# Optimization experiments

Measured on AMD Instinct MI355X. Metric: run time of the kernel, lower is better.

The kernel has to match this reference:

```python
import math
import jax, jax.numpy as jnp
import numpy as np
from jax import lax

RAY_START, RAY_END = 0.5, 2.5
N_PLANES = 32

# ---- camera constants (faithful to pose_spherical / fibonacci_sphere / ImagePlanes init) ----

def _pose_spherical_np(theta, phi, radius):
    trans_t = np.array([[1,0,0,0],[0,1,0,0],[0,0,1,radius],[0,0,0,1]], dtype=np.float64)
    p = phi/180.0*np.pi
    rot_phi = np.array([[1,0,0,0],[0,np.cos(p),-np.sin(p),0],[0,np.sin(p),np.cos(p),0],[0,0,0,1]], dtype=np.float64)
    t = theta/180.0*np.pi
    rot_theta = np.array([[np.cos(t),0,-np.sin(t),0],[0,1,0,0],[np.sin(t),0,np.cos(t),0],[0,0,0,1]], dtype=np.float64)
    e = 90.0/180.0*np.pi
    rot_eta = np.array([[np.cos(e),np.sin(e),0,0],[-np.sin(e),np.cos(e),0,0],[0,0,1,0],[0,0,0,1]], dtype=np.float64)
    c2w = rot_eta @ (rot_theta @ (rot_phi @ trans_t))
    return np.array([[-1,0,0,0],[0,0,1,0],[0,1,0,0],[0,0,0,1]], dtype=np.float64) @ c2w

def _fibonacci_sphere(n):
    pts = []
    golden = math.pi*(math.sqrt(5.0)-1.0)
    for i in range(n):
        y = 1 - (i/float(n-1))*2
        r = math.sqrt(1-y*y)
        th = golden*i
        x, z = math.cos(th)*r, math.sin(th)*r
        pts.append((math.atan2(z, math.sqrt(x*x+y*y)), math.atan2(y, x)))
    return pts

_poses = np.stack([_pose_spherical_np(theta, phi, -1.307) for phi, theta in _fibonacci_sphere(N_PLANES)])
_flip = np.diag(np.array([-1.0,1.0,1.0,1.0]))
POSES34 = jnp.asarray(np.stack([np.linalg.inv(p @ _flip)[:3] for p in _poses]).astype(np.float32))  # [32,3,4]
KMAT = jnp.asarray(np.array([[1.0254,0,0.5],[0,1.0254,0.5],[0,0,1]], dtype=np.float32))  # [3,3]

# ---- grid_sample(bilinear, zeros, align_corners=False) ----

def _grid_sample(img, grid):
    # img [C,H,W], grid [P,2] (x,y) in [-1,1] -> [C,P]
    C, H, W = img.shape
    ix = ((grid[:, 0] + 1.0)*W - 1.0)*0.5
    iy = ((grid[:, 1] + 1.0)*H - 1.0)*0.5
    x0 = jnp.floor(ix); y0 = jnp.floor(iy)
    wx1 = ix - x0; wy1 = iy - y0
    def tap(xx, yy, w):
        valid = (xx >= 0) & (xx <= W - 1) & (yy >= 0) & (yy <= H - 1)
        xi = jnp.clip(xx, 0, W - 1).astype(jnp.int32)
        yi = jnp.clip(yy, 0, H - 1).astype(jnp.int32)
        return img[:, yi, xi] * (w*valid)[None, :]
    return (tap(x0, y0, (1-wx1)*(1-wy1)) + tap(x0+1, y0, wx1*(1-wy1))
            + tap(x0, y0+1, (1-wx1)*wy1) + tap(x0+1, y0+1, wx1*wy1))

# ---- ImagePlanes.forward ----

def _image_plane_feats(images, points):
    # images [32,3,H,W], points [P,3] -> [P, 96+64]
    P = points.shape[0]
    ph = jnp.concatenate([points, jnp.ones((P, 1), points.dtype)], axis=1)  # [P,4]
    cam = jnp.einsum('kij,pj->kip', POSES34, ph)            # [32,3,P]
    ps = jnp.einsum('ij,kjp->kip', KMAT, cam)                # [32,3,P]
    pix = jnp.clip(ps[:, :2, :] / ps[:, 2:3, :], 0.0, 1.0)*2.0 - 1.0  # [32,2,P]
    grid = jnp.transpose(pix, (0, 2, 1))                     # [32,P,2]
    feats = jax.vmap(_grid_sample)(images, grid)             # [32,3,P]
    feats = jnp.transpose(feats, (2, 0, 1)).reshape(P, -1)   # [P,96] plane-major
    pixflat = jnp.transpose(grid, (1, 0, 2)).reshape(P, -1)  # [P,64]
    return jnp.concatenate([feats, pixflat], axis=1)

# ---- RenderNetwork.forward (only self.net path is used) ----

def _decode(x, W1, b1, W2, b2):
    h = jax.nn.softplus(x @ W1 + b1)
    o = h @ W2 + b2
    rgb = jax.nn.sigmoid(o[..., 1:])*(1.0 + 2*0.001) - 0.001
    return rgb, o[..., 0:1]

# ---- MipRayMarcher2 ----

def _ray_march(colors, densities, depths):
    deltas = depths[:, :, 1:] - depths[:, :, :-1]
    cm = (colors[:, :, :-1] + colors[:, :, 1:])*0.5
    dm = (densities[:, :, :-1] + densities[:, :, 1:])*0.5
    zm = (depths[:, :, :-1] + depths[:, :, 1:])*0.5
    dm = jax.nn.softplus(dm - 1.0)
    alpha = 1.0 - jnp.exp(-dm*deltas)
    shifted = jnp.concatenate([jnp.ones_like(alpha[:, :, :1]), 1.0 - alpha + 1e-10], axis=2)
    weights = alpha * jnp.cumprod(shifted, axis=2)[:, :, :-1]
    rgb = jnp.sum(weights*cm, axis=2)*2.0 - 1.0
    wtot = jnp.sum(weights, axis=2)
    depth = jnp.sum(weights*zm, axis=2)/wtot
    depth = jnp.clip(jnp.where(jnp.isnan(depth), jnp.inf, depth), jnp.min(depths), jnp.max(depths))
    return rgb, depth, weights

# ---- importance sampling (sample_pdf + maxpool/avgpool smoothing) ----

def _sample_pdf(bins, weights, u, eps=1e-5):
    M = weights.shape[-1]
    weights = weights + eps
    pdf = weights / jnp.sum(weights, -1, keepdims=True)
    cdf = jnp.cumsum(pdf, -1)
    cdf = jnp.concatenate([jnp.zeros_like(cdf[:, :1]), cdf], -1)  # [R,M+1]
    inds = jax.vmap(lambda c, uu: jnp.searchsorted(c, uu, side='right'))(cdf, u)
    below = jnp.maximum(inds - 1, 0)
    above = jnp.minimum(inds, M)
    cdf_b = jnp.take_along_axis(cdf, below, 1)
    cdf_a = jnp.take_along_axis(cdf, above, 1)
    bins_b = jnp.take_along_axis(bins, below, 1)
    bins_a = jnp.take_along_axis(bins, above, 1)
    denom = jnp.where(cdf_a - cdf_b < eps, 1.0, cdf_a - cdf_b)
    return bins_b + (u - cdf_b)/denom*(bins_a - bins_b)

def _sample_importance(z_vals, weights, n_imp, u):
    B, N, S, _ = z_vals.shape
    z = z_vals.reshape(B*N, S)
    w = weights.reshape(B*N, S - 1)
    wp = jnp.pad(w, ((0, 0), (1, 1)), constant_values=-jnp.inf)
    m = jnp.maximum(wp[:, :-1], wp[:, 1:])          # max_pool1d(k=2,s=1,p=1)
    sm = (m[:, :-1] + m[:, 1:])*0.5 + 0.01           # avg_pool1d(k=2,s=1)
    samples = _sample_pdf(z, sm[:, 1:-1], u.reshape(B*N, n_imp))
    return lax.stop_gradient(samples).reshape(B, N, n_imp, 1)

# ---- full ImportanceRenderer.forward ----

def _forward(planes, ray_origins, ray_directions, strat_noise, pdf_u, W1, b1, W2, b2, D, n_imp):
    B, N = ray_origins.shape[0], ray_origins.shape[1]
    H, Wd = planes.shape[-2], planes.shape[-1]
    images = planes.reshape(B, N_PLANES, 3, H, Wd)
    delta = (RAY_END - RAY_START)/(D - 1)
    depths_c = jnp.linspace(RAY_START, RAY_END, D, dtype=planes.dtype).reshape(1, 1, D, 1) + strat_noise*delta

    def run_pass(depths):
        S = depths.shape[2]
        pts = (ray_origins[:, :, None, :] + depths*ray_directions[:, :, None, :]).reshape(B, N*S, 3)
        feats = jax.vmap(_image_plane_feats)(images, pts)  # [B,N*S,160]
        rgb, sigma = _decode(feats, W1, b1, W2, b2)
        return rgb.reshape(B, N, S, 32), sigma.reshape(B, N, S, 1)

    colors_c, dens_c = run_pass(depths_c)
    _, _, w_c = _ray_march(colors_c, dens_c, depths_c)
    depths_f = _sample_importance(depths_c, w_c, n_imp, pdf_u)
    colors_f, dens_f = run_pass(depths_f)

    all_d = jnp.concatenate([depths_c, depths_f], axis=2)
    all_c = jnp.concatenate([colors_c, colors_f], axis=2)
    all_s = jnp.concatenate([dens_c, dens_f], axis=2)
    order = jnp.argsort(all_d[..., 0], axis=2)[..., None]
    all_d = jnp.take_along_axis(all_d, order, axis=2)
    all_c = jnp.take_along_axis(all_c, order, axis=2)
    all_s = jnp.take_along_axis(all_s, order, axis=2)
    rgb_final, depth_final, w = _ray_march(all_c, all_s, all_d)
    return jnp.concatenate([rgb_final, depth_final, jnp.sum(w, axis=2)], axis=-1)  # [B,N,34]


def setup_inputs() -> dict:
    key = jax.random.key(0)
    ks = jax.random.split(key, 7)
    B, N, D, NI, H = 2, 4096, 48, 48, 64
    rd = jax.random.normal(ks[2], (B, N, 3), jnp.float32)
    rd = rd / jnp.linalg.norm(rd, axis=-1, keepdims=True)
    return {
        'planes': jax.random.normal(ks[0], (B, 96, H, H), jnp.float32),
        'ray_origins': jax.random.normal(ks[1], (B, N, 3), jnp.float32)*0.1,
        'ray_directions': rd,
        'strat_noise': jax.random.uniform(ks[3], (B, N, D, 1), jnp.float32),
        'pdf_u': jax.random.uniform(ks[4], (B, N, NI), jnp.float32),
        'W1': jax.random.normal(ks[5], (160, 64), jnp.float32)*0.05,
        'b1': jnp.zeros((64,), jnp.float32),
        'W2': jax.random.normal(ks[6], (64, 33), jnp.float32)*0.05,
        'b2': jnp.zeros((33,), jnp.float32),
        'depth_resolution': 48,
        'N_importance': 48,
    }


def reference(planes, ray_origins, ray_directions, strat_noise, pdf_u, W1, b1, W2, b2, depth_resolution, N_importance):
    return _forward(planes, ray_origins, ray_directions, strat_noise, pdf_u, W1, b1, W2, b2, depth_resolution, N_importance)
```

## Files before the change

kernel.cpp:

```cpp
#include <hip/hip_runtime.h>
#include <math.h>

#define B_   2
#define N_   4096
#define S_   48
#define NPL  32
#define NRAYS (B_*N_)
#define NPTS  (NRAYS*S_)
#define DELTA_ (2.0f/47.0f)
#define NBLK_FUSED (NPTS/256)

#define ST_XS    65
#define ST_YS    66
#define ST_PLANE (ST_YS*ST_XS)
#define SETUP_GRID 258

#define OFF_POSES  0
#define OFF_MINMAX 384
#define OFF_W1E    512
#define OFF_W2E    8704
#define OFF_B2E    10240
#define OFF_ST     16384
#define OFF_DC     1114624
#define OFF_DF     1507840
#define OFF_SC     1901056
#define OFF_SF     2294272
#define OFF_CC     2687488
#define OFF_CF     8978944

typedef __attribute__((ext_vector_type(8))) short short8;
typedef __attribute__((ext_vector_type(4))) float f32x4;
typedef __attribute__((ext_vector_type(2))) float f32x2;

__device__ __forceinline__ float softplus_f(float x) {
    return fmaxf(x, 0.f) + __logf(1.f + __expf(-fabsf(x)));
}
__device__ __forceinline__ float sigmoid_f(float x) {
    return __builtin_amdgcn_rcpf(1.f + __expf(-x));
}
__device__ __forceinline__ unsigned short bf16rne(float x) {
    unsigned u = __float_as_uint(x);
    u += 0x7FFFu + ((u >> 16) & 1u);
    return (unsigned short)(u >> 16);
}
__device__ __forceinline__ unsigned bf16pk(float lo, float hi) {
    return (unsigned)bf16rne(lo) | ((unsigned)bf16rne(hi) << 16);
}
__device__ __forceinline__ float bf2f(unsigned short v) {
    return __uint_as_float(((unsigned)v) << 16);
}
__device__ __forceinline__ float bflo(unsigned u) { return __uint_as_float(u << 16); }
__device__ __forceinline__ float bfhi(unsigned u) { return __uint_as_float(u & 0xffff0000u); }
__device__ __forceinline__ f32x2 unpk2(unsigned u) { return (f32x2){bflo(u), bfhi(u)}; }
__device__ __forceinline__ int div48(int pt) {
    return (int)(((unsigned)(pt >> 4) * 43691u) >> 17);
}

__device__ void mul3(const double* a, const double* b, double* o) {
    for (int i = 0; i < 3; i++)
        for (int j = 0; j < 3; j++) {
            double s = 0.0;
            for (int k = 0; k < 3; k++) s += a[i*3+k]*b[k*3+j];
            o[i*3+j] = s;
        }
}

__global__ __launch_bounds__(256) void k_setup(
    float* ws, const float* __restrict__ W1,
    const float* __restrict__ W2, const float* __restrict__ b2,
    const float* __restrict__ planes, const float* __restrict__ noise)
{
    __shared__ unsigned short texs[3][4096];
    __shared__ float smn[4], smx[4];
    int bid = blockIdx.x;
    int t = threadIdx.x;
    if (bid == 0) {
        if (t < 32) {
            double y = 1.0 - (t/31.0)*2.0;
            double rr = sqrt(fmax(1.0 - y*y, 0.0));
            double golden = M_PI*(sqrt(5.0) - 1.0);
            double th = golden*(double)t;
            double x = cos(th)*rr, z = sin(th)*rr;
            double phi   = atan2(z, sqrt(x*x + y*y));
            double theta = atan2(y, x);
            double p  = phi/180.0*M_PI;
            double tt = theta/180.0*M_PI;
            double e  = 90.0/180.0*M_PI;
            double cp = cos(p), sp = sin(p), ct = cos(tt), st = sin(tt);
            double ce = cos(e), se = sin(e);
            double Ph[9] = {1,0,0,  0,cp,-sp,  0,sp,cp};
            double Th[9] = {ct,0,-st,  0,1,0,  st,0,ct};
            double Et[9] = {ce,se,0,  -se,ce,0,  0,0,1};
            double M3[9] = {-1,0,0,  0,0,1,  0,1,0};
            double A[9], Bm[9], R[9];
            mul3(Th, Ph, A);
            mul3(Et, A, Bm);
            mul3(M3, Bm, R);
            double radius = -1.307;
            double tv0 = radius*R[2], tv1 = radius*R[5], tv2 = radius*R[8];
            double Rf[9] = {-R[0],R[1],R[2], -R[3],R[4],R[5], -R[6],R[7],R[8]};
            float rowv[3][4];
            for (int j = 0; j < 3; j++) {
                double r0 = Rf[0*3+j], r1 = Rf[1*3+j], r2 = Rf[2*3+j];
                rowv[j][0] = (float)r0;
                rowv[j][1] = (float)r1;
                rowv[j][2] = (float)r2;
                rowv[j][3] = (float)(-(r0*tv0 + r1*tv1 + r2*tv2));
            }
            float* P = ws + OFF_POSES + t*12;
            P[0] = rowv[0][0]; P[1] = rowv[1][0];
            P[2] = rowv[0][1]; P[3] = rowv[1][1];
            P[4] = rowv[0][2]; P[5] = rowv[1][2];
            P[6] = rowv[0][3]; P[7] = rowv[1][3];
            P[8] = rowv[2][0]; P[9] = rowv[2][1]; P[10] = rowv[2][2]; P[11] = rowv[2][3];
        }
        unsigned short* w1e = (unsigned short*)(ws + OFF_W1E);
        for (int o = t; o < 64*256; o += 256) {
            int chunk = o >> 9, lane = (o >> 3) & 63, j = o & 7;
            int s = chunk >> 2, nt = chunk & 3, q = lane >> 4, n = lane & 15;
            int nn = nt*16 + n;
            int p = s*4 + q;
            float v = 0.f;
            if (j < 3)      v = W1[(3*p+j)*64 + nn];
            else if (j < 5) v = W1[(96 + 2*p + (j-3))*64 + nn];
            w1e[o] = bf16rne(v);
        }
        unsigned short* w2e = (unsigned short*)(ws + OFF_W2E);
        for (int o = t; o < 6*512; o += 256) {
            int chunk = o >> 9, lane = (o >> 3) & 63, j = o & 7;
            int nt = chunk >> 1, s2 = chunk & 1, q = lane >> 4, n = lane & 15;
            int nn = nt*16 + n;
            int k2 = s2*32 + q*8 + j;
            float v = (nn < 33) ? W2[k2*33 + nn] : 0.f;
            w2e[o] = bf16rne(v);
        }
        for (int idx = t; idx < 48; idx += 256)
            ws[OFF_B2E + idx] = (idx < 33) ? b2[idx] : 0.f;
    } else if (bid == 1) {
        float mn = 1e30f, mx = -1e30f;
        for (int r = t; r < NRAYS; r += 256) {
            float n0  = noise[(size_t)r*48];
            float n47 = noise[(size_t)r*48 + 47];
            mn = fminf(mn, 0.5f + n0*DELTA_);
            mx = fmaxf(mx, 0.5f + 47.f*DELTA_ + n47*DELTA_);
        }
        for (int off = 32; off > 0; off >>= 1) {
            mn = fminf(mn, __shfl_down(mn, off));
            mx = fmaxf(mx, __shfl_down(mx, off));
        }
        if ((t & 63) == 0) { smn[t >> 6] = mn; smx[t >> 6] = mx; }
        __syncthreads();
        if (t == 0) {
            ws[OFF_MINMAX]     = fminf(fminf(smn[0], smn[1]), fminf(smn[2], smn[3]));
            ws[OFF_MINMAX + 1] = fmaxf(fmaxf(smx[0], smx[1]), fmaxf(smx[2], smx[3]));
        }
    } else {
        int idx = bid - 2;
        int bp = idx >> 2, part = idx & 3;
        int b = bp >> 5, p = bp & 31;
        const float* base = planes + ((size_t)b*96 + 3*p)*4096;
        for (int i = t; i < 4096; i += 256) {
            texs[0][i] = bf16rne(base[i]);
            texs[1][i] = bf16rne(base[4096 + i]);
            texs[2][i] = bf16rne(base[8192 + i]);
        }
        __syncthreads();
        uint4* qd = (uint4*)(ws + OFF_ST) + (size_t)bp*ST_PLANE;
        int e0 = part*1073, e1 = min(ST_PLANE, e0 + 1073);
        for (int e = e0 + t; e < e1; e += 256) {
            int y = e / ST_XS, x = e - y*ST_XS;
            int jy = y - 1;
            unsigned a01 = 0, a2 = 0, b01 = 0, b2v = 0;
            if (jy >= 0 && jy <= 63) {
                int jxa = x - 1, jxb = x;
                if (jxa >= 0 && jxa <= 63) {
                    int ti = jy*64 + jxa;
                    a01 = (unsigned)texs[0][ti] | ((unsigned)texs[1][ti] << 16);
                    a2  = (unsigned)texs[2][ti];
                }
                if (jxb <= 63) {
                    int ti = jy*64 + jxb;
                    b01 = (unsigned)texs[0][ti] | ((unsigned)texs[1][ti] << 16);
                    b2v = (unsigned)texs[2][ti];
                }
            }
            qd[e] = make_uint4(a01, a2, b01, b2v);
        }
    }
}

__device__ __forceinline__ void proj_pt(
    const f32x2 Px, const f32x2 Py, const f32x2 Pz, const f32x2 Pw, const f32x4 Pc,
    float px, float py, float pz,
    int& eoff, float& wx, float& wy, unsigned& gpk)
{
    f32x2 c01 = Pz*pz + Pw;
    c01 = Py*py + c01;
    c01 = Px*px + c01;
    float c2 = fmaf(Pc.x,px, fmaf(Pc.y,py, fmaf(Pc.z,pz, Pc.w)));
    float rz = __builtin_amdgcn_rcpf(c2);
    f32x2 t01 = c01*1.0254f + 0.5f*c2;
    t01 = t01*rz;
    float cx = fminf(fmaxf(t01.x, 0.f), 1.f);
    float cy = fminf(fmaxf(t01.y, 0.f), 1.f);
    float gx = fmaf(2.f, cx, -1.f);
    float gy = fmaf(2.f, cy, -1.f);
    float ixp = fmaf(64.f, cx, 0.5f);
    float iyp = fmaf(64.f, cy, 0.5f);
    float xf = floorf(ixp), yf = floorf(iyp);
    wx = ixp - xf; wy = iyp - yf;
    eoff = (int)yf*ST_XS + (int)xf;
    gpk = bf16pk(gx, gy);
}

__device__ __forceinline__ void bilerp_pack(
    const uint4 r0, const uint4 r1, float wx, float wy, unsigned gpk, uint4& av)
{
    float wy0 = 1.f - wy, wy1 = wy;
    float w0x = 1.f - wx, w1x = wx;
    f32x2 tl01 = unpk2(r0.x)*wy0 + unpk2(r1.x)*wy1;
    float tl2  = fmaf(wy0, bflo(r0.y), wy1*bflo(r1.y));
    f32x2 tr01 = unpk2(r0.z)*wy0 + unpk2(r1.z)*wy1;
    float tr2  = fmaf(wy0, bflo(r0.w), wy1*bflo(r1.w));
    f32x2 f01 = tl01*w0x + tr01*w1x;
    float f2  = fmaf(w0x, tl2, w1x*tr2);
    av.x = bf16pk(f01.x, f01.y);
    av.y = ((unsigned)bf16rne(f2)) | (gpk << 16);
    av.z = gpk >> 16;
    av.w = 0u;
}

__global__ __launch_bounds__(512, 4) void k_fused(
    const uint4* __restrict__ stq, const float* __restrict__ poses,
    const float* __restrict__ b1, const unsigned short* __restrict__ w1e,
    const unsigned short* __restrict__ w2e, const float* __restrict__ b2e,
    unsigned short* __restrict__ colors, float* __restrict__ dens,
    const float* __restrict__ noise, const float* __restrict__ ro,
    const float* __restrict__ rd, const float* __restrict__ u,
    float* __restrict__ ws, int coarse)
{
    __shared__ __align__(16) unsigned short w1s[16384];
    __shared__ __align__(16) unsigned short w2s[3072];
    __shared__ __align__(16) unsigned short smem[8][1152];
    __shared__ __align__(16) float pl[384];
    __shared__ float impz[6][48];
    __shared__ float impcdf[6][46];
    __shared__ __align__(16) float4 posl[6][48];
    int tid = threadIdx.x;
    int wv = tid >> 6, lane = tid & 63;
    int n = lane & 15, q = lane >> 4;
    int bid = blockIdx.x;
    int swz = (bid & 7)*(NBLK_FUSED/8) + (bid >> 3);
    int wlocal = swz*256 + wv*32;
    int bq = (swz*256 >= NPTS/2) ? 32 : 0;
    int r0 = (int)(((unsigned)(swz*16) * 43691u) >> 17);

    {
        const uint4* g1 = (const uint4*)w1e;
        uint4* d1 = (uint4*)w1s;
        for (int i = tid; i < 2048; i += 512) d1[i] = g1[i];
        const uint4* g2 = (const uint4*)w2e;
        uint4* d2 = (uint4*)w2s;
        if (tid < 384) { d2[tid] = g2[tid]; pl[tid] = poses[tid]; }
    }

    if (!coarse && wv < 6) {
        int r = r0 + wv;
        const float* z   = ws + OFF_DC + (size_t)r*48;
        const float* den = ws + OFF_SC + (size_t)r*48;
        float zv = 0.f, dv = 0.f;
        if (lane < 48) { zv = z[lane]; dv = den[lane]; impz[wv][lane] = zv; }
        float zn  = __shfl_down(zv, 1);
        float dnn = __shfl_down(dv, 1);
        float alpha = 0.f, f = 1.f;
        if (lane < 47) {
            float sp = softplus_f(0.5f*(dv + dnn) - 1.f);
            alpha = 1.f - __expf(-sp*(zn - zv));
            f = 1.f - alpha + 1e-10f;
        }
        float v = f;
        for (int off = 1; off < 64; off <<= 1) { float o = __shfl_up(v, off); if (lane >= off) v *= o; }
        float T = __shfl_up(v, 1); if (lane == 0) T = 1.f;
        float w = alpha*T;
        float wn1 = __shfl_down(w, 1), wn2 = __shfl_down(w, 2);
        float pw = 0.f;
        if (lane < 45) pw = 0.5f*(fmaxf(w, wn1) + fmaxf(wn1, wn2)) + 0.01f + 1e-5f;
        float s = pw;
        for (int off = 1; off < 64; off <<= 1) { float o = __shfl_up(s, off); if (lane >= off) s += o; }
        float csum = __shfl(s, 63);
        if (lane < 45) impcdf[wv][lane+1] = s/csum;
        if (lane == 63) impcdf[wv][0] = 0.f;
        if (lane < 48) {
            float uu = u[(size_t)r*48 + lane];
            int lo = 0, hi = 46;
            while (lo < hi) { int mid = (lo+hi)>>1; if (uu >= impcdf[wv][mid]) lo = mid+1; else hi = mid; }
            int below = max(lo-1, 0), above = min(lo, 45);
            float cb = impcdf[wv][below], ca = impcdf[wv][above];
            float zb = impz[wv][below],   za = impz[wv][above];
            float dn2 = ca - cb; if (dn2 < 1e-5f) dn2 = 1.f;
            float df_s = zb + (uu - cb)/dn2*(za - zb);
            ws[OFF_DF + (size_t)r*48 + lane] = df_s;
            float fx = fmaf(df_s, rd[r*3+0], ro[r*3+0]);
            float fy = fmaf(df_s, rd[r*3+1], ro[r*3+1]);
            float fz = fmaf(df_s, rd[r*3+2], ro[r*3+2]);
            posl[wv][lane] = make_float4(fx, fy, fz, df_s);
        }
    }
    __syncthreads();

    float px[2], py[2], pz[2];
    if (coarse) {
#pragma unroll
        for (int t = 0; t < 2; t++) {
            int pt = wlocal + t*16 + n;
            int ray = div48(pt);
            int j = pt - ray*48;
            float depth = 0.5f + (float)j*DELTA_ + noise[pt]*DELTA_;
            px[t] = fmaf(depth, rd[ray*3+0], ro[ray*3+0]);
            py[t] = fmaf(depth, rd[ray*3+1], ro[ray*3+1]);
            pz[t] = fmaf(depth, rd[ray*3+2], ro[ray*3+2]);
            if (q == 0) ws[OFF_DC + pt] = depth;
        }
    } else {
#pragma unroll
        for (int t = 0; t < 2; t++) {
            int pt = wlocal + t*16 + n;
            int ray = div48(pt);
            float4 pv = posl[ray - r0][pt - ray*48];
            px[t] = pv.x; py[t] = pv.y; pz[t] = pv.z;
        }
    }

    f32x4 acc[2][4];
#pragma unroll
    for (int t = 0; t < 2; t++)
#pragma unroll
        for (int nt = 0; nt < 4; nt++) {
            float bv = b1[nt*16 + n];
            acc[t][nt] = (f32x4){bv, bv, bv, bv};
        }

#pragma unroll
    for (int s = 0; s < 8; s++) {
        int plane = s*4 + q;
        const float* Pp = pl + plane*12;
        f32x2 Px = *(const f32x2*)(Pp);
        f32x2 Py = *(const f32x2*)(Pp + 2);
        f32x2 Pz = *(const f32x2*)(Pp + 4);
        f32x2 Pw = *(const f32x2*)(Pp + 6);
        f32x4 Pc = *(const f32x4*)(Pp + 8);
        const uint4* stp = stq + (unsigned)(bq + plane)*(unsigned)ST_PLANE;
        union { short8 s8; uint4 u; } av[2];
        {
            int eo0, eo1; float wx0, wy0, wx1, wy1; unsigned g0, g1;
            proj_pt(Px, Py, Pz, Pw, Pc, px[0], py[0], pz[0], eo0, wx0, wy0, g0);
            proj_pt(Px, Py, Pz, Pw, Pc, px[1], py[1], pz[1], eo1, wx1, wy1, g1);
            uint4 a0 = stp[eo0], a1 = stp[eo0 + ST_XS];
            uint4 b0 = stp[eo1], b1r = stp[eo1 + ST_XS];
            bilerp_pack(a0, a1, wx0, wy0, g0, av[0].u);
            bilerp_pack(b0, b1r, wx1, wy1, g1, av[1].u);
        }
#pragma unroll
        for (int nt = 0; nt < 4; nt++) {
            short8 bfw = *(const short8*)(w1s + ((s*4 + nt) << 9) + (lane << 3));
#pragma unroll
            for (int t = 0; t < 2; t++)
                acc[t][nt] = __builtin_amdgcn_mfma_f32_16x16x32_bf16(av[t].s8, bfw, acc[t][nt], 0, 0, 0);
        }
    }

    short8 b2f[3][2];
#pragma unroll
    for (int nt = 0; nt < 3; nt++)
#pragma unroll
        for (int s2 = 0; s2 < 2; s2++)
            b2f[nt][s2] = *(const short8*)(w2s + (((nt << 1) | s2) << 9) + (lane << 3));

    unsigned short* ht = &smem[wv][0];
#pragma unroll
    for (int t = 0; t < 2; t++) {
#pragma unroll
        for (int nt = 0; nt < 4; nt++)
#pragma unroll
            for (int r = 0; r < 4; r++) {
                float hv = softplus_f(acc[t][nt][r]);
                ht[(q*4 + r)*72 + nt*16 + n] = bf16rne(hv);
            }
        short8 a2[2];
#pragma unroll
        for (int s2 = 0; s2 < 2; s2++)
            a2[s2] = *(const short8*)(ht + n*72 + s2*32 + q*8);

        f32x4 acc2[3];
#pragma unroll
        for (int nt = 0; nt < 3; nt++) {
            float bv = b2e[nt*16 + n];
            acc2[nt] = (f32x4){bv, bv, bv, bv};
        }
#pragma unroll
        for (int nt = 0; nt < 3; nt++)
#pragma unroll
            for (int s2 = 0; s2 < 2; s2++)
                acc2[nt] = __builtin_amdgcn_mfma_f32_16x16x32_bf16(a2[s2], b2f[nt][s2], acc2[nt], 0, 0, 0);

        float* ot = (float*)ht;
#pragma unroll
        for (int nt = 0; nt < 3; nt++) {
            int col = nt*16 + n;
#pragma unroll
            for (int r = 0; r < 4; r++) {
                float v = acc2[nt][r];
                int row = q*4 + r;
                if (col == 0) ot[row*34 + 32] = v;
                else if (col <= 32) {
                    float sg = sigmoid_f(v);
                    ot[row*34 + (col-1)] = fmaf(sg, 1.002f, -0.001f);
                }
            }
        }
        unsigned* cgu = (unsigned*)(colors + (size_t)(wlocal + t*16)*32);
#pragma unroll
        for (int i = 0; i < 4; i++) {
            int ui = i*64 + lane;
            int pt = ui >> 4, ch = (ui & 15)*2;
            cgu[ui] = bf16pk(ot[pt*34 + ch], ot[pt*34 + ch + 1]);
        }
        if (lane < 16) dens[wlocal + t*16 + lane] = ot[lane*34 + 32];
    }
}

__global__ __launch_bounds__(256) void k_final(float* __restrict__ out, const float* __restrict__ ws,
                                               const unsigned short* __restrict__ cC,
                                               const unsigned short* __restrict__ cF)
{
    __shared__ float kd[4][96];
    __shared__ float kden[4][96];
    __shared__ float sdl[4][96];
    __shared__ float sdenl[4][96];
    __shared__ int   sidxl[4][96];
    __shared__ float warr[4][96];
    __shared__ float earr[4][96];
    int tid = threadIdx.x;
    int wv = tid >> 6, lane = tid & 63;
    int r = blockIdx.x*4 + wv;
    const float* dc = ws + OFF_DC + (size_t)r*48;
    const float* df = ws + OFF_DF + (size_t)r*48;
    const float* sc = ws + OFF_SC + (size_t)r*48;
    const float* sf = ws + OFF_SF + (size_t)r*48;
    for (int i = lane; i < 96; i += 64) {
        float d, dn;
        if (i < 48) { d = dc[i]; dn = sc[i]; }
        else        { d = df[i-48]; dn = sf[i-48]; }
        kd[wv][i] = d; kden[wv][i] = dn;
    }
    __syncthreads();
    for (int i = lane; i < 96; i += 64) {
        float d = kd[wv][i];
        int rank = 0;
        for (int j = 0; j < 96; j++) {
            float dj = kd[wv][j];
            rank += (int)((dj < d) | ((dj == d) & (j < i)));
        }
        sdl[wv][rank] = d; sdenl[wv][rank] = kden[wv][i]; sidxl[wv][rank] = i;
    }
    __syncthreads();
    int i2 = 2*lane;
    float a0=0.f, f0=1.f, a1=0.f, f1=1.f, d0=0.f, d1=0.f, d2=0.f;
    if (i2 < 95) {
        d0 = sdl[wv][i2]; d1 = sdl[wv][i2+1];
        float sp = softplus_f(0.5f*(sdenl[wv][i2] + sdenl[wv][i2+1]) - 1.f);
        a0 = 1.f - __expf(-sp*(d1 - d0)); f0 = 1.f - a0 + 1e-10f;
    }
    if (i2+1 < 95) {
        d2 = sdl[wv][i2+2];
        float sp = softplus_f(0.5f*(sdenl[wv][i2+1] + sdenl[wv][i2+2]) - 1.f);
        a1 = 1.f - __expf(-sp*(d2 - d1)); f1 = 1.f - a1 + 1e-10f;
    }
    float p = f0*f1, v = p;
    for (int off = 1; off < 64; off <<= 1) { float o = __shfl_up(v, off); if (lane >= off) v *= o; }
    float excl = __shfl_up(v, 1); if (lane == 0) excl = 1.f;
    float w0 = a0*excl, w1 = a1*excl*f0;
    if (i2   < 96) warr[wv][i2]   = w0;
    if (i2+1 < 96) warr[wv][i2+1] = w1;
    float wsm = w0 + w1;
    float dsm = w0*0.5f*(d0+d1) + w1*0.5f*(d1+d2);
    for (int off = 32; off; off >>= 1) { wsm += __shfl_xor(wsm, off); dsm += __shfl_xor(dsm, off); }
    __syncthreads();
    for (int i = lane; i < 96; i += 64) {
        float wp = (i > 0)  ? warr[wv][i-1] : 0.f;
        float wc = (i < 95) ? warr[wv][i]   : 0.f;
        earr[wv][sidxl[wv][i]] = 0.5f*(wp + wc);
    }
    __syncthreads();
    int ch = lane & 31, half = lane >> 5;
    const unsigned short* cbase = (half ? cF : cC) + ((size_t)r*48)*32 + ch;
    const float* eb = &earr[wv][half*48];
    float a = 0.f;
    for (int jj = 0; jj < 48; jj++)
        a = fmaf(eb[jj], bf2f(cbase[(size_t)jj*32]), a);
    a += __shfl_xor(a, 32);
    if (lane < 32) out[(size_t)r*34 + lane] = 2.f*a - 1.f;
    if (lane == 0) {
        float gmn = ws[OFF_MINMAX];
        float gmx = ws[OFF_MINMAX + 1];
        float depth = dsm/wsm;
        if (depth != depth) depth = __builtin_inff();
        depth = fminf(fmaxf(depth, gmn), gmx);
        out[(size_t)r*34 + 32] = depth;
        out[(size_t)r*34 + 33] = wsm;
    }
}

extern "C" void kernel_launch(void* const* d_in, const int* in_sizes, int n_in,
                              void* d_out, int out_size, void* d_ws, size_t ws_size,
                              hipStream_t stream) {
    const float* planes = (const float*)d_in[0];
    const float* ro     = (const float*)d_in[1];
    const float* rd     = (const float*)d_in[2];
    const float* noise  = (const float*)d_in[3];
    const float* u      = (const float*)d_in[4];
    const float* W1     = (const float*)d_in[5];
    const float* b1     = (const float*)d_in[6];
    const float* W2     = (const float*)d_in[7];
    const float* b2     = (const float*)d_in[8];
    float* ws  = (float*)d_ws;
    float* out = (float*)d_out;
    const unsigned short* w1e = (const unsigned short*)(ws + OFF_W1E);
    const unsigned short* w2e = (const unsigned short*)(ws + OFF_W2E);
    const uint4* stq = (const uint4*)(ws + OFF_ST);
    unsigned short* cC = (unsigned short*)(ws + OFF_CC);
    unsigned short* cF = (unsigned short*)(ws + OFF_CF);

    hipLaunchKernelGGL(k_setup, dim3(SETUP_GRID), dim3(256), 0, stream,
                       ws, W1, W2, b2, planes, noise);
    hipLaunchKernelGGL(k_fused, dim3(NBLK_FUSED), dim3(512), 0, stream,
                       stq, ws + OFF_POSES, b1, w1e, w2e, ws + OFF_B2E, cC, ws + OFF_SC,
                       noise, ro, rd, u, ws, 1);
    hipLaunchKernelGGL(k_fused, dim3(NBLK_FUSED), dim3(512), 0, stream,
                       stq, ws + OFF_POSES, b1, w1e, w2e, ws + OFF_B2E, cF, ws + OFF_SF,
                       noise, ro, rd, u, ws, 0);
    hipLaunchKernelGGL(k_final, dim3(NRAYS/4), dim3(256), 0, stream, out, ws, cC, cF);
}
```

Baseline: 223.4 us.

## Shrink LDS footprint by aliasing scratch buffers and raise occupancy target

Merges the per-wave hidden-activation scratch with the importance-sampling buffers (posl, impz, impcdf) into one aliased LDS region, separated by an extra barrier. It also drops the LDS copy of W2 so second-layer weight fragments load straight from global memory, and raises the launch-bounds minimum blocks per CU from 4 to 6. The aim is to cut LDS per block so more blocks fit on each CU and hide latency better. The risks are extra register pressure from the tighter bound, possible spills, and an added barrier.

```diff
diff --git a/kernel.cpp b/kernel.cpp
--- a/kernel.cpp
+++ b/kernel.cpp
@@ -230,7 +230,7 @@
     av.w = 0u;
 }
 
-__global__ __launch_bounds__(512, 4) void k_fused(
+__global__ __launch_bounds__(512, 6) void k_fused(
     const uint4* __restrict__ stq, const float* __restrict__ poses,
     const float* __restrict__ b1, const unsigned short* __restrict__ w1e,
     const unsigned short* __restrict__ w2e, const float* __restrict__ b2e,
@@ -240,12 +240,11 @@
     float* __restrict__ ws, int coarse)
 {
     __shared__ __align__(16) unsigned short w1s[16384];
-    __shared__ __align__(16) unsigned short w2s[3072];
-    __shared__ __align__(16) unsigned short smem[8][1152];
+    __shared__ __align__(16) float uni[4608];
     __shared__ __align__(16) float pl[384];
-    __shared__ float impz[6][48];
-    __shared__ float impcdf[6][46];
-    __shared__ __align__(16) float4 posl[6][48];
+    float4* posl  = (float4*)uni;
+    float*  impz  = uni + 1152;
+    float*  impcdf= uni + 1440;
     int tid = threadIdx.x;
     int wv = tid >> 6, lane = tid & 63;
     int n = lane & 15, q = lane >> 4;
@@ -259,9 +258,7 @@
         const uint4* g1 = (const uint4*)w1e;
         uint4* d1 = (uint4*)w1s;
         for (int i = tid; i < 2048; i += 512) d1[i] = g1[i];
-        const uint4* g2 = (const uint4*)w2e;
-        uint4* d2 = (uint4*)w2s;
-        if (tid < 384) { d2[tid] = g2[tid]; pl[tid] = poses[tid]; }
+        if (tid < 384) pl[tid] = poses[tid];
     }
 
     if (!coarse && wv < 6) {
@@ -269,7 +266,7 @@
         const float* z   = ws + OFF_DC + (size_t)r*48;
         const float* den = ws + OFF_SC + (size_t)r*48;
         float zv = 0.f, dv = 0.f;
-        if (lane < 48) { zv = z[lane]; dv = den[lane]; impz[wv][lane] = zv; }
+        if (lane < 48) { zv = z[lane]; dv = den[lane]; impz[wv*48 + lane] = zv; }
         float zn  = __shfl_down(zv, 1);
         float dnn = __shfl_down(dv, 1);
         float alpha = 0.f, f = 1.f;
@@ -288,22 +285,22 @@
         float s = pw;
         for (int off = 1; off < 64; off <<= 1) { float o = __shfl_up(s, off); if (lane >= off) s += o; }
         float csum = __shfl(s, 63);
-        if (lane < 45) impcdf[wv][lane+1] = s/csum;
-        if (lane == 63) impcdf[wv][0] = 0.f;
+        if (lane < 45) impcdf[wv*46 + lane+1] = s/csum;
+        if (lane == 63) impcdf[wv*46] = 0.f;
         if (lane < 48) {
             float uu = u[(size_t)r*48 + lane];
             int lo = 0, hi = 46;
-            while (lo < hi) { int mid = (lo+hi)>>1; if (uu >= impcdf[wv][mid]) lo = mid+1; else hi = mid; }
+            while (lo < hi) { int mid = (lo+hi)>>1; if (uu >= impcdf[wv*46 + mid]) lo = mid+1; else hi = mid; }
             int below = max(lo-1, 0), above = min(lo, 45);
-            float cb = impcdf[wv][below], ca = impcdf[wv][above];
-            float zb = impz[wv][below],   za = impz[wv][above];
+            float cb = impcdf[wv*46 + below], ca = impcdf[wv*46 + above];
+            float zb = impz[wv*48 + below],   za = impz[wv*48 + above];
             float dn2 = ca - cb; if (dn2 < 1e-5f) dn2 = 1.f;
             float df_s = zb + (uu - cb)/dn2*(za - zb);
             ws[OFF_DF + (size_t)r*48 + lane] = df_s;
             float fx = fmaf(df_s, rd[r*3+0], ro[r*3+0]);
             float fy = fmaf(df_s, rd[r*3+1], ro[r*3+1]);
             float fz = fmaf(df_s, rd[r*3+2], ro[r*3+2]);
-            posl[wv][lane] = make_float4(fx, fy, fz, df_s);
+            posl[wv*48 + lane] = make_float4(fx, fy, fz, df_s);
         }
     }
     __syncthreads();
@@ -326,10 +323,11 @@
         for (int t = 0; t < 2; t++) {
             int pt = wlocal + t*16 + n;
             int ray = div48(pt);
-            float4 pv = posl[ray - r0][pt - ray*48];
+            float4 pv = posl[(ray - r0)*48 + (pt - ray*48)];
             px[t] = pv.x; py[t] = pv.y; pz[t] = pv.z;
         }
     }
+    __syncthreads();
 
     f32x4 acc[2][4];
 #pragma unroll
@@ -374,9 +372,9 @@
     for (int nt = 0; nt < 3; nt++)
 #pragma unroll
         for (int s2 = 0; s2 < 2; s2++)
-            b2f[nt][s2] = *(const short8*)(w2s + (((nt << 1) | s2) << 9) + (lane << 3));
-
-    unsigned short* ht = &smem[wv][0];
+            b2f[nt][s2] = *(const short8*)(w2e + (((nt << 1) | s2) << 9) + (lane << 3));
+
+    unsigned short* ht = (unsigned short*)uni + wv*1152;
 #pragma unroll
     for (int t = 0; t < 2; t++) {
 #pragma unroll
```

Result: slower. 228.6 us (+2.3%).
